# Kernel tuning notes

Measured on AMD Instinct MI355X. Metric: run time of the kernel, lower is better.

The kernel has to match this reference:

```python
import jax, jax.numpy as jnp
import numpy as np

D = 2048
N_PASSES = 2
TOKENS = 16384


def _wht_matrix(d):
    # Sylvester construction of the (unnormalized) Walsh-Hadamard matrix.
    h = np.array([[1.0]], dtype=np.float32)
    while h.shape[0] < d:
        h = np.block([[h, h], [h, -h]])
    return jnp.asarray(h)


def setup_inputs() -> dict:
    key = jax.random.key(0)
    kx, ks = jax.random.split(key)
    x = jax.random.normal(kx, (TOKENS, D), dtype=jnp.float32)
    # random +/-1 sign arrays, one per pass (buffers in the torch module)
    signs = (2 * jax.random.randint(ks, (N_PASSES, D), 0, 2) - 1).astype(jnp.int32)
    wht_mat = _wht_matrix(D)
    return {"x": x, "signs": signs, "wht_mat": wht_mat}


def reference(x, signs, wht_mat):
    # Cascaded SRHT: (sign flip -> dense WHT matmul) x n_passes, scale fused at end.
    final_scale = jnp.asarray(1.0 / (D ** (N_PASSES / 2.0)), dtype=x.dtype)
    s = signs.astype(x.dtype)
    out = x
    for i in range(N_PASSES):
        out = out * s[i]          # [tokens, d] broadcast sign flip
        out = out @ wht_mat       # [tokens, d] x [d, d]
    return out * final_scale
```

## Files before the change

### kernel.cpp

```cpp
#include <hip/hip_runtime.h>

#define DIM 2048

__device__ __forceinline__ int sw(int e) {
  return e ^ (((e >> 7) & 7) << 2);
}

__device__ __forceinline__ float4 sign_flip(float4 v, uint4 s) {
  float4 r;
  r.x = __uint_as_float(__float_as_uint(v.x) ^ (s.x & 0x80000000u));
  r.y = __uint_as_float(__float_as_uint(v.y) ^ (s.y & 0x80000000u));
  r.z = __uint_as_float(__float_as_uint(v.z) ^ (s.z & 0x80000000u));
  r.w = __uint_as_float(__float_as_uint(v.w) ^ (s.w & 0x80000000u));
  return r;
}

#define BFLY(a, b) { float _t = (a); (a) = _t + (b); (b) = _t - (b); }

__device__ __forceinline__ void bf4_pair(float4 &a, float4 &b) {
  BFLY(a.x, b.x); BFLY(a.y, b.y); BFLY(a.z, b.z); BFLY(a.w, b.w);
}

__device__ __forceinline__ void bf_comps(float4 &a) {
  BFLY(a.x, a.y); BFLY(a.z, a.w);
  BFLY(a.x, a.z); BFLY(a.y, a.w);
}

__device__ __forceinline__ void bf_oct(float4 v[8]) {
  bf4_pair(v[0], v[1]); bf4_pair(v[2], v[3]);
  bf4_pair(v[4], v[5]); bf4_pair(v[6], v[7]);
  bf4_pair(v[0], v[2]); bf4_pair(v[1], v[3]);
  bf4_pair(v[4], v[6]); bf4_pair(v[5], v[7]);
  bf4_pair(v[0], v[4]); bf4_pair(v[1], v[5]);
  bf4_pair(v[2], v[6]); bf4_pair(v[3], v[7]);
}

template <int CTRL>
__device__ __forceinline__ float dpp_mov(float x) {
  return __int_as_float(
      __builtin_amdgcn_mov_dpp(__float_as_int(x), CTRL, 0xF, 0xF, true));
}

template <int CTRL>
__device__ __forceinline__ void dpp_stage(float4 v[8], float sgn) {
  #pragma unroll
  for (int i = 0; i < 8; ++i) {
    float px = dpp_mov<CTRL>(v[i].x);
    float py = dpp_mov<CTRL>(v[i].y);
    float pz = dpp_mov<CTRL>(v[i].z);
    float pw = dpp_mov<CTRL>(v[i].w);
    v[i].x = fmaf(sgn, v[i].x, px);
    v[i].y = fmaf(sgn, v[i].y, py);
    v[i].z = fmaf(sgn, v[i].z, pz);
    v[i].w = fmaf(sgn, v[i].w, pw);
  }
}

__global__ __launch_bounds__(256) void srht2_kernel(
    const float* __restrict__ x, const int* __restrict__ signs,
    float* __restrict__ out, int nrows) {
  __shared__ __align__(16) float lds[4][DIM];
  const int lane = threadIdx.x & 63;
  const int wv   = threadIdx.x >> 6;
  const int row  = blockIdx.x * 4 + wv;

  const float sgn1 = (lane & 1) ? -1.0f : 1.0f;
  const float sgn2 = (lane & 2) ? -1.0f : 1.0f;

  const float4* __restrict__ xr = (const float4*)(x + (size_t)row * DIM);
  const uint4*  __restrict__ s0 = (const uint4*)signs;

  float4 v[8];
  #pragma unroll
  for (int c = 0; c < 8; ++c) v[c] = xr[c * 64 + lane];
  #pragma unroll
  for (int c = 0; c < 8; ++c) v[c] = sign_flip(v[c], s0[c * 64 + lane]);

  #pragma unroll
  for (int c = 0; c < 8; ++c) bf_comps(v[c]);
  bf_oct(v);
  dpp_stage<0xB1>(v, sgn1);
  dpp_stage<0x4E>(v, sgn2);

  float* L = lds[wv];
  #pragma unroll
  for (int c = 0; c < 8; ++c)
    *(float4*)(L + sw(c * 256 + lane * 4)) = v[c];
  __syncthreads();

  const int rbase = (((lane >> 1) & 1) << 2) | (((lane >> 2) & 1) << 3)
                  | ((lane & 1) << 7) | ((lane >> 3) << 8);
  float4 w[8];
  #pragma unroll
  for (int j = 0; j < 8; ++j)
    w[j] = *(const float4*)(L + sw(rbase + (j << 4)));

  bf_oct(w);
  dpp_stage<0xB1>(w, sgn1);

  const uint4* __restrict__ s1 = (const uint4*)(signs + DIM);
  #pragma unroll
  for (int j = 0; j < 8; ++j)
    w[j] = sign_flip(w[j], s1[(rbase >> 2) + (j << 2)]);

  #pragma unroll
  for (int j = 0; j < 8; ++j) bf_comps(w[j]);
  bf_oct(w);
  dpp_stage<0xB1>(w, sgn1);
  dpp_stage<0x4E>(w, sgn2);

  __syncthreads();
  #pragma unroll
  for (int j = 0; j < 8; ++j)
    *(float4*)(L + sw(rbase + (j << 4))) = w[j];
  __syncthreads();

  const int rb2 = ((lane & 1) << 3) | (((lane >> 1) & 1) << 2)
                | (((lane >> 2) & 1) << 4) | (((lane >> 3) & 1) << 5)
                | (((lane >> 4) & 1) << 6) | (((lane >> 5) & 1) << 7);
  #pragma unroll
  for (int c = 0; c < 8; ++c)
    v[c] = *(const float4*)(L + sw(rb2 + (c << 8)));

  bf_oct(v);
  dpp_stage<0xB1>(v, sgn1);

  const float sc = 1.0f / 2048.0f;
  float4* __restrict__ orow = (float4*)(out + (size_t)row * DIM);
  #pragma unroll
  for (int c = 0; c < 8; ++c) {
    float4 t = v[c];
    t.x *= sc; t.y *= sc; t.z *= sc; t.w *= sc;
    orow[(rb2 >> 2) + (c << 6)] = t;
  }
}

extern "C" void kernel_launch(void* const* d_in, const int* in_sizes, int n_in,
                              void* d_out, int out_size, void* d_ws, size_t ws_size,
                              hipStream_t stream) {
  const float* x     = (const float*)d_in[0];
  const int*   signs = (const int*)d_in[1];
  float*       out   = (float*)d_out;
  const int nrows   = in_sizes[0] / DIM;
  const int nblocks = nrows / 4;
  hipLaunchKernelGGL(srht2_kernel, dim3(nblocks), dim3(256), 0, stream,
                     x, signs, out, nrows);
}
```

Baseline: 238.2 us.

## Process two rows per wave and replace block barriers with LDS waitcnt fences

Each wavefront now transforms two rows, interleaving their butterfly stages and sharing the sign loads, and the grid is halved to match. Block-wide __syncthreads are replaced by s_waitcnt lgkmcnt(0) fences, since each wave only uses its own LDS slice. Launch bounds now request 4 blocks per CU. The aim is more independent work per wave to hide memory and DPP latency and to drop barrier stalls, at the cost of higher register pressure and fewer waves in flight. Correctness relies on intra-wave LDS ordering being enough without a barrier.

```diff
diff --git a/kernel.cpp b/kernel.cpp
--- a/kernel.cpp
+++ b/kernel.cpp
@@ -56,82 +56,117 @@
   }
 }
 
-__global__ __launch_bounds__(256) void srht2_kernel(
+__device__ __forceinline__ void lds_fence() {
+  asm volatile("s_waitcnt lgkmcnt(0)" ::: "memory");
+}
+
+__global__ __launch_bounds__(256, 4) void srht2_kernel(
     const float* __restrict__ x, const int* __restrict__ signs,
     float* __restrict__ out, int nrows) {
   __shared__ __align__(16) float lds[4][DIM];
   const int lane = threadIdx.x & 63;
   const int wv   = threadIdx.x >> 6;
-  const int row  = blockIdx.x * 4 + wv;
+  const int row0 = (blockIdx.x * 4 + wv) * 2;
 
   const float sgn1 = (lane & 1) ? -1.0f : 1.0f;
   const float sgn2 = (lane & 2) ? -1.0f : 1.0f;
 
-  const float4* __restrict__ xr = (const float4*)(x + (size_t)row * DIM);
-  const uint4*  __restrict__ s0 = (const uint4*)signs;
+  const float4* __restrict__ xr0 = (const float4*)(x + (size_t)row0 * DIM);
+  const float4* __restrict__ xr1 = xr0 + DIM / 4;
+  const uint4*  __restrict__ s0  = (const uint4*)signs;
 
-  float4 v[8];
+  float4 a[8], b[8];
   #pragma unroll
-  for (int c = 0; c < 8; ++c) v[c] = xr[c * 64 + lane];
+  for (int c = 0; c < 8; ++c) {
+    a[c] = xr0[c * 64 + lane];
+    b[c] = xr1[c * 64 + lane];
+  }
   #pragma unroll
-  for (int c = 0; c < 8; ++c) v[c] = sign_flip(v[c], s0[c * 64 + lane]);
+  for (int c = 0; c < 8; ++c) {
+    const uint4 s = s0[c * 64 + lane];
+    a[c] = sign_flip(a[c], s);
+    b[c] = sign_flip(b[c], s);
+  }
 
   #pragma unroll
-  for (int c = 0; c < 8; ++c) bf_comps(v[c]);
-  bf_oct(v);
-  dpp_stage<0xB1>(v, sgn1);
-  dpp_stage<0x4E>(v, sgn2);
+  for (int c = 0; c < 8; ++c) { bf_comps(a[c]); bf_comps(b[c]); }
+  bf_oct(a); bf_oct(b);
+  dpp_stage<0xB1>(a, sgn1); dpp_stage<0xB1>(b, sgn1);
+  dpp_stage<0x4E>(a, sgn2); dpp_stage<0x4E>(b, sgn2);
 
   float* L = lds[wv];
+  const int rbase = (((lane >> 1) & 1) << 2) | (((lane >> 2) & 1) << 3)
+                  | ((lane & 1) << 7) | ((lane >> 3) << 8);
+
+  float4 wa[8], wb[8];
   #pragma unroll
   for (int c = 0; c < 8; ++c)
-    *(float4*)(L + sw(c * 256 + lane * 4)) = v[c];
-  __syncthreads();
-
-  const int rbase = (((lane >> 1) & 1) << 2) | (((lane >> 2) & 1) << 3)
-                  | ((lane & 1) << 7) | ((lane >> 3) << 8);
-  float4 w[8];
+    *(float4*)(L + sw(c * 256 + lane * 4)) = a[c];
+  lds_fence();
   #pragma unroll
   for (int j = 0; j < 8; ++j)
-    w[j] = *(const float4*)(L + sw(rbase + (j << 4)));
+    wa[j] = *(const float4*)(L + sw(rbase + (j << 4)));
+  lds_fence();
+  #pragma unroll
+  for (int c = 0; c < 8; ++c)
+    *(float4*)(L + sw(c * 256 + lane * 4)) = b[c];
+  lds_fence();
+  #pragma unroll
+  for (int j = 0; j < 8; ++j)
+    wb[j] = *(const float4*)(L + sw(rbase + (j << 4)));
 
-  bf_oct(w);
-  dpp_stage<0xB1>(w, sgn1);
+  bf_oct(wa); bf_oct(wb);
+  dpp_stage<0xB1>(wa, sgn1); dpp_stage<0xB1>(wb, sgn1);
 
   const uint4* __restrict__ s1 = (const uint4*)(signs + DIM);
   #pragma unroll
-  for (int j = 0; j < 8; ++j)
-    w[j] = sign_flip(w[j], s1[(rbase >> 2) + (j << 2)]);
+  for (int j = 0; j < 8; ++j) {
+    const uint4 s = s1[(rbase >> 2) + (j << 2)];
+    wa[j] = sign_flip(wa[j], s);
+    wb[j] = sign_flip(wb[j], s);
+  }
 
   #pragma unroll
-  for (int j = 0; j < 8; ++j) bf_comps(w[j]);
-  bf_oct(w);
-  dpp_stage<0xB1>(w, sgn1);
-  dpp_stage<0x4E>(w, sgn2);
-
-  __syncthreads();
-  #pragma unroll
-  for (int j = 0; j < 8; ++j)
-    *(float4*)(L + sw(rbase + (j << 4))) = w[j];
-  __syncthreads();
+  for (int j = 0; j < 8; ++j) { bf_comps(wa[j]); bf_comps(wb[j]); }
+  bf_oct(wa); bf_oct(wb);
+  dpp_stage<0xB1>(wa, sgn1); dpp_stage<0xB1>(wb, sgn1);
+  dpp_stage<0x4E>(wa, sgn2); dpp_stage<0x4E>(wb, sgn2);
 
   const int rb2 = ((lane & 1) << 3) | (((lane >> 1) & 1) << 2)
                 | (((lane >> 2) & 1) << 4) | (((lane >> 3) & 1) << 5)
                 | (((lane >> 4) & 1) << 6) | (((lane >> 5) & 1) << 7);
+
+  lds_fence();
+  #pragma unroll
+  for (int j = 0; j < 8; ++j)
+    *(float4*)(L + sw(rbase + (j << 4))) = wa[j];
+  lds_fence();
   #pragma unroll
   for (int c = 0; c < 8; ++c)
-    v[c] = *(const float4*)(L + sw(rb2 + (c << 8)));
+    a[c] = *(const float4*)(L + sw(rb2 + (c << 8)));
+  lds_fence();
+  #pragma unroll
+  for (int j = 0; j < 8; ++j)
+    *(float4*)(L + sw(rbase + (j << 4))) = wb[j];
+  lds_fence();
+  #pragma unroll
+  for (int c = 0; c < 8; ++c)
+    b[c] = *(const float4*)(L + sw(rb2 + (c << 8)));
 
-  bf_oct(v);
-  dpp_stage<0xB1>(v, sgn1);
+  bf_oct(a); bf_oct(b);
+  dpp_stage<0xB1>(a, sgn1); dpp_stage<0xB1>(b, sgn1);
 
   const float sc = 1.0f / 2048.0f;
-  float4* __restrict__ orow = (float4*)(out + (size_t)row * DIM);
+  float4* __restrict__ orow0 = (float4*)(out + (size_t)row0 * DIM);
+  float4* __restrict__ orow1 = orow0 + DIM / 4;
   #pragma unroll
   for (int c = 0; c < 8; ++c) {
-    float4 t = v[c];
-    t.x *= sc; t.y *= sc; t.z *= sc; t.w *= sc;
-    orow[(rb2 >> 2) + (c << 6)] = t;
+    float4 ta = a[c];
+    ta.x *= sc; ta.y *= sc; ta.z *= sc; ta.w *= sc;
+    orow0[(rb2 >> 2) + (c << 6)] = ta;
+    float4 tb = b[c];
+    tb.x *= sc; tb.y *= sc; tb.z *= sc; tb.w *= sc;
+    orow1[(rb2 >> 2) + (c << 6)] = tb;
   }
 }
 
@@ -142,7 +177,7 @@
   const int*   signs = (const int*)d_in[1];
   float*       out   = (float*)d_out;
   const int nrows   = in_sizes[0] / DIM;
-  const int nblocks = nrows / 4;
+  const int nblocks = nrows / 8;
   hipLaunchKernelGGL(srht2_kernel, dim3(nblocks), dim3(256), 0, stream,
                      x, signs, out, nrows);
 }
```

After: 261.2 us. 1.1x slower.

## Replace LDS transposes with in-register ds_swizzle and permlane32 butterflies

Applied to the files above, without the earlier changes.

Computes every WHT stage within registers and across lanes. It uses DPP for lane distances 1 and 2, ds_swizzle for 4, 8 and 16, and permlane32_swap for 32, then finishes with the register octet butterflies. This removes the shared-memory round trips, the block-wide syncs and the permuted index layouts, so loads and stores become fully coalesced in natural order. The launch-bounds occupancy hint is also raised. The cost is more cross-lane shuffle instructions per stage, and ds_swizzle still goes through the LDS pipeline.

```diff
diff --git a/kernel.cpp b/kernel.cpp
--- a/kernel.cpp
+++ b/kernel.cpp
@@ -2,9 +2,7 @@
 
 #define DIM 2048
 
-__device__ __forceinline__ int sw(int e) {
-  return e ^ (((e >> 7) & 7) << 2);
-}
+typedef unsigned int uint2v __attribute__((ext_vector_type(2)));
 
 __device__ __forceinline__ float4 sign_flip(float4 v, uint4 s) {
   float4 r;
@@ -56,74 +54,90 @@
   }
 }
 
-__global__ __launch_bounds__(256) void srht2_kernel(
+template <int PAT>
+__device__ __forceinline__ float swz_mov(float x) {
+  return __int_as_float(__builtin_amdgcn_ds_swizzle(__float_as_int(x), PAT));
+}
+
+template <int PAT>
+__device__ __forceinline__ void swz_stage(float4 v[8], float sgn) {
+  #pragma unroll
+  for (int i = 0; i < 8; ++i) {
+    float px = swz_mov<PAT>(v[i].x);
+    float py = swz_mov<PAT>(v[i].y);
+    float pz = swz_mov<PAT>(v[i].z);
+    float pw = swz_mov<PAT>(v[i].w);
+    v[i].x = fmaf(sgn, v[i].x, px);
+    v[i].y = fmaf(sgn, v[i].y, py);
+    v[i].z = fmaf(sgn, v[i].z, pz);
+    v[i].w = fmaf(sgn, v[i].w, pw);
+  }
+}
+
+__device__ __forceinline__ float pl32_bfly(float x, float sgn) {
+  uint2v r = __builtin_amdgcn_permlane32_swap(
+      __float_as_uint(x), __float_as_uint(x), false, false);
+  return fmaf(sgn, __uint_as_float(r[1]), __uint_as_float(r[0]));
+}
+
+__device__ __forceinline__ void pl32_stage(float4 v[8], float sgn) {
+  #pragma unroll
+  for (int i = 0; i < 8; ++i) {
+    v[i].x = pl32_bfly(v[i].x, sgn);
+    v[i].y = pl32_bfly(v[i].y, sgn);
+    v[i].z = pl32_bfly(v[i].z, sgn);
+    v[i].w = pl32_bfly(v[i].w, sgn);
+  }
+}
+
+__global__ __launch_bounds__(256, 8) void srht2_kernel(
     const float* __restrict__ x, const int* __restrict__ signs,
     float* __restrict__ out, int nrows) {
-  __shared__ __align__(16) float lds[4][DIM];
   const int lane = threadIdx.x & 63;
   const int wv   = threadIdx.x >> 6;
   const int row  = blockIdx.x * 4 + wv;
+  if (row >= nrows) return;
 
-  const float sgn1 = (lane & 1) ? -1.0f : 1.0f;
-  const float sgn2 = (lane & 2) ? -1.0f : 1.0f;
+  const float sgn1  = (lane & 1)  ? -1.0f : 1.0f;
+  const float sgn2  = (lane & 2)  ? -1.0f : 1.0f;
+  const float sgn4  = (lane & 4)  ? -1.0f : 1.0f;
+  const float sgn8  = (lane & 8)  ? -1.0f : 1.0f;
+  const float sgn16 = (lane & 16) ? -1.0f : 1.0f;
+  const float sgn32 = (lane & 32) ? -1.0f : 1.0f;
 
   const float4* __restrict__ xr = (const float4*)(x + (size_t)row * DIM);
   const uint4*  __restrict__ s0 = (const uint4*)signs;
+  const uint4*  __restrict__ s1 = (const uint4*)(signs + DIM);
 
   float4 v[8];
   #pragma unroll
-  for (int c = 0; c < 8; ++c) v[c] = xr[c * 64 + lane];
-  #pragma unroll
-  for (int c = 0; c < 8; ++c) v[c] = sign_flip(v[c], s0[c * 64 + lane]);
+  for (int c = 0; c < 8; ++c) {
+    v[c] = xr[c * 64 + lane];
+    v[c] = sign_flip(v[c], s0[c * 64 + lane]);
+  }
 
   #pragma unroll
   for (int c = 0; c < 8; ++c) bf_comps(v[c]);
-  bf_oct(v);
   dpp_stage<0xB1>(v, sgn1);
   dpp_stage<0x4E>(v, sgn2);
-
-  float* L = lds[wv];
-  #pragma unroll
-  for (int c = 0; c < 8; ++c)
-    *(float4*)(L + sw(c * 256 + lane * 4)) = v[c];
-  __syncthreads();
-
-  const int rbase = (((lane >> 1) & 1) << 2) | (((lane >> 2) & 1) << 3)
-                  | ((lane & 1) << 7) | ((lane >> 3) << 8);
-  float4 w[8];
-  #pragma unroll
-  for (int j = 0; j < 8; ++j)
-    w[j] = *(const float4*)(L + sw(rbase + (j << 4)));
-
-  bf_oct(w);
-  dpp_stage<0xB1>(w, sgn1);
-
-  const uint4* __restrict__ s1 = (const uint4*)(signs + DIM);
-  #pragma unroll
-  for (int j = 0; j < 8; ++j)
-    w[j] = sign_flip(w[j], s1[(rbase >> 2) + (j << 2)]);
+  swz_stage<0x101F>(v, sgn4);
+  swz_stage<0x201F>(v, sgn8);
+  swz_stage<0x401F>(v, sgn16);
+  pl32_stage(v, sgn32);
+  bf_oct(v);
 
   #pragma unroll
-  for (int j = 0; j < 8; ++j) bf_comps(w[j]);
-  bf_oct(w);
-  dpp_stage<0xB1>(w, sgn1);
-  dpp_stage<0x4E>(w, sgn2);
+  for (int c = 0; c < 8; ++c) v[c] = sign_flip(v[c], s1[c * 64 + lane]);
 
-  __syncthreads();
   #pragma unroll
-  for (int j = 0; j < 8; ++j)
-    *(float4*)(L + sw(rbase + (j << 4))) = w[j];
-  __syncthreads();
-
-  const int rb2 = ((lane & 1) << 3) | (((lane >> 1) & 1) << 2)
-                | (((lane >> 2) & 1) << 4) | (((lane >> 3) & 1) << 5)
-                | (((lane >> 4) & 1) << 6) | (((lane >> 5) & 1) << 7);
-  #pragma unroll
-  for (int c = 0; c < 8; ++c)
-    v[c] = *(const float4*)(L + sw(rb2 + (c << 8)));
-
+  for (int c = 0; c < 8; ++c) bf_comps(v[c]);
+  dpp_stage<0xB1>(v, sgn1);
+  dpp_stage<0x4E>(v, sgn2);
+  swz_stage<0x101F>(v, sgn4);
+  swz_stage<0x201F>(v, sgn8);
+  swz_stage<0x401F>(v, sgn16);
+  pl32_stage(v, sgn32);
   bf_oct(v);
-  dpp_stage<0xB1>(v, sgn1);
 
   const float sc = 1.0f / 2048.0f;
   float4* __restrict__ orow = (float4*)(out + (size_t)row * DIM);
@@ -131,7 +145,7 @@
   for (int c = 0; c < 8; ++c) {
     float4 t = v[c];
     t.x *= sc; t.y *= sc; t.z *= sc; t.w *= sc;
-    orow[(rb2 >> 2) + (c << 6)] = t;
+    orow[c * 64 + lane] = t;
   }
 }
 
```

Result: slower. 265.7 us (+11.6%).
